# Kernel optimization log

Hardware: AMD Instinct MI355X
Metric: run time of the kernel (lower is better)

The kernel has to match this reference:

```python
import jax, jax.numpy as jnp
import numpy as np

N = 8192      # num nodes
E = 8192      # num hyperedges
D = 256       # embedding dim
DENSITY = 0.01
LEAKY = 0.2   # negative_slope of LeakyReLU


def setup_inputs() -> dict:
    key = jax.random.key(0)
    k1, k2, k3, k4, k5 = jax.random.split(key, 5)
    # sparse adjacency matrices represented densely (values * bernoulli mask)
    inp_adj = jax.random.normal(k1, (E, N), dtype=jnp.float32) * (
        jax.random.uniform(k2, (E, N)) < DENSITY
    ).astype(jnp.float32)
    att_adj = jax.random.normal(k3, (N, E), dtype=jnp.float32) * (
        jax.random.uniform(k4, (N, E)) < DENSITY
    ).astype(jnp.float32)
    embs = jax.random.normal(k5, (N, D), dtype=jnp.float32)
    return {"inp_adj": inp_adj, "att_adj": att_adj, "embs": embs}


def reference(inp_adj, att_adj, embs):
    # adj = att_adj @ inp_adj  (spgemm in the original)  -> [N, N]
    adj = att_adj @ inp_adj
    # adj @ (adj.T @ embs)  (two spmm)  -> [N, D]
    out = adj @ (adj.T @ embs)
    # LeakyReLU(negative_slope=LEAKY)
    return jnp.where(out > 0, out, LEAKY * out)
```

## Files before the change

kernel.cpp:

```cpp
#include <hip/hip_runtime.h>
#include <stdint.h>

#define NROWS 8192
#define NCOLS 8192
#define DDIM  256
#define SLOTS 160
#define SCRN  192
#define CAP   786432
#define HB    128
#define RPB   (NROWS / HB)

__device__ __forceinline__ float bf16lo(uint32_t u) { return __uint_as_float(u << 16); }
__device__ __forceinline__ float bf16hi(uint32_t u) { return __uint_as_float(u & 0xffff0000u); }
__device__ __forceinline__ uint32_t f2bf(float f) {
    uint32_t b = __float_as_uint(f);
    return (b + 0x7fffu + ((b >> 16) & 1u)) >> 16;
}

__global__ __launch_bounds__(256) void cvt_kernel(const float* __restrict__ in,
                                                  uint32_t* __restrict__ out) {
    int i = blockIdx.x * 256 + threadIdx.x;
    float2 f = ((const float2*)in)[i];
    out[i] = f2bf(f.x) | (f2bf(f.y) << 16);
}

__device__ __forceinline__ void emit_nz(float v, uint32_t col, int& base,
                                        uint2* __restrict__ s) {
    unsigned long long m = __ballot(v != 0.f);
    if (m) {
        if (v != 0.f) {
            int pre = __builtin_amdgcn_mbcnt_hi((uint32_t)(m >> 32),
                      __builtin_amdgcn_mbcnt_lo((uint32_t)m, 0u));
            int o = base + pre;
            if (o < SCRN) s[o] = make_uint2(col, __float_as_uint(v));
        }
        base += (int)__popcll(m);
    }
}

template<int CH>
__device__ __forceinline__ void process_chunk(const float4 (&d)[8], int lane,
                                              int& base, uint2* __restrict__ s) {
    #pragma unroll
    for (int i = 0; i < 8; ++i) {
        const uint32_t cbase = (uint32_t)((CH * 512 + i * 64 + lane) * 4);
        emit_nz(d[i].x, cbase + 0, base, s);
        emit_nz(d[i].y, cbase + 1, base, s);
        emit_nz(d[i].z, cbase + 2, base, s);
        emit_nz(d[i].w, cbase + 3, base, s);
    }
}

__global__ __launch_bounds__(256) void extract_kernel(
        const float* __restrict__ MA, const float* __restrict__ MB,
        int* __restrict__ rcA, uint2* __restrict__ pairA,
        int* __restrict__ rcB, uint2* __restrict__ pairB) {
    __shared__ uint2 scr[4][SCRN];
    const int wv   = threadIdx.x >> 6;
    const int lane = threadIdx.x & 63;
    const int W = blockIdx.x * 4 + wv;
    const int which = W >> 13;
    const int r = W & (NROWS - 1);
    const float* __restrict__ M = which ? MB : MA;
    int*   rc     = which ? rcB : rcA;
    uint2* g_pair = which ? pairB : pairA;

    const float4* __restrict__ M4 = (const float4*)(M + (size_t)r * NCOLS);
    uint2* __restrict__ dst = g_pair + (size_t)r * SLOTS;
    uint2* __restrict__ s = scr[wv];

    float4 da[8], db[8];
    #pragma unroll
    for (int i = 0; i < 8; ++i) da[i] = M4[0 * 512 + i * 64 + lane];
    #pragma unroll
    for (int i = 0; i < 8; ++i) db[i] = M4[1 * 512 + i * 64 + lane];
    __builtin_amdgcn_sched_barrier(0);

    int base = 0;
    process_chunk<0>(da, lane, base, s);
    #pragma unroll
    for (int i = 0; i < 8; ++i) da[i] = M4[2 * 512 + i * 64 + lane];
    __builtin_amdgcn_sched_barrier(0);
    process_chunk<1>(db, lane, base, s);
    #pragma unroll
    for (int i = 0; i < 8; ++i) db[i] = M4[3 * 512 + i * 64 + lane];
    __builtin_amdgcn_sched_barrier(0);
    process_chunk<2>(da, lane, base, s);
    process_chunk<3>(db, lane, base, s);

    const int n = base < SLOTS ? base : SLOTS;
    for (int j = lane; j < n; j += 64) dst[j] = s[j];
    if (lane == 0) rc[r] = n;
}

__global__ __launch_bounds__(256) void hist_kernel(
        const int* __restrict__ rcA, const uint2* __restrict__ pairA, int* __restrict__ PA,
        const int* __restrict__ rcB, const uint2* __restrict__ pairB, int* __restrict__ PB) {
    const int which = blockIdx.x >> 7;
    const int b = blockIdx.x & (HB - 1);
    const int* rc      = which ? rcB : rcA;
    const uint2* pair  = which ? pairB : pairA;
    int* P = which ? PB : PA;
    __shared__ int h[NCOLS];
    const int tid = threadIdx.x;
    const int wv = tid >> 6, lane = tid & 63;
    for (int i = tid; i < NCOLS; i += 256) h[i] = 0;
    __syncthreads();
    for (int r = b * RPB + wv; r < (b + 1) * RPB; r += 4) {
        const int c = rc[r];
        const uint2* __restrict__ p = pair + (size_t)r * SLOTS;
        for (int j = lane; j < c; j += 64) atomicAdd(&h[p[j].x], 1);
    }
    __syncthreads();
    for (int i = tid; i < NCOLS; i += 256) P[b * NCOLS + i] = h[i];
}

__global__ __launch_bounds__(256) void coltot_kernel(
        const int* __restrict__ PA, int* __restrict__ totA,
        const int* __restrict__ PB, int* __restrict__ totB) {
    const int which = blockIdx.x >> 5;
    const int cb = blockIdx.x & 31;
    const int* P = which ? PB : PA;
    int* tot = which ? totB : totA;
    const int c = cb * 256 + threadIdx.x;
    int sum = 0;
    #pragma unroll 8
    for (int b = 0; b < HB; ++b) sum += P[b * NCOLS + c];
    tot[c] = sum;
}

__global__ __launch_bounds__(256) void prefix_kernel(
        const int* __restrict__ totA, int* __restrict__ startA,
        const int* __restrict__ totB, int* __restrict__ startB) {
    const int* cnt = blockIdx.x ? totB : totA;
    int* start     = blockIdx.x ? startB : startA;
    __shared__ int wtot[4];
    const int tid = threadIdx.x;
    const int wv = tid >> 6, lane = tid & 63;
    const int chunk = NCOLS / 256;
    const int base = tid * chunk;
    int sum = 0;
    for (int i = 0; i < chunk; ++i) sum += cnt[base + i];
    int inc = sum;
    #pragma unroll
    for (int sd = 1; sd < 64; sd <<= 1) {
        int t = __shfl_up(inc, sd, 64);
        if (lane >= sd) inc += t;
    }
    if (lane == 63) wtot[wv] = inc;
    __syncthreads();
    if (tid == 0) {
        int acc = 0;
        #pragma unroll
        for (int i = 0; i < 4; ++i) { int t = wtot[i]; wtot[i] = acc; acc += t; }
    }
    __syncthreads();
    int run = wtot[wv] + inc - sum;
    for (int i = 0; i < chunk; ++i) { start[base + i] = run; run += cnt[base + i]; }
}

__global__ __launch_bounds__(256) void offsets_kernel(
        int* __restrict__ PA, const int* __restrict__ startA,
        int* __restrict__ PB, const int* __restrict__ startB) {
    const int which = blockIdx.x >> 5;
    const int cb = blockIdx.x & 31;
    int* P = which ? PB : PA;
    const int* start = which ? startB : startA;
    const int c = cb * 256 + threadIdx.x;
    int run = start[c];
    for (int b = 0; b < HB; ++b) {
        int t = P[b * NCOLS + c];
        P[b * NCOLS + c] = run;
        run += t;
    }
}

__global__ __launch_bounds__(256) void scatter_kernel(
        const int* __restrict__ rcA, const uint2* __restrict__ pairA,
        const int* __restrict__ PA, uint2* __restrict__ cscA,
        const int* __restrict__ rcB, const uint2* __restrict__ pairB,
        const int* __restrict__ PB, uint2* __restrict__ cscB) {
    const int which = blockIdx.x >> 7;
    const int b = blockIdx.x & (HB - 1);
    const int* rc     = which ? rcB : rcA;
    const uint2* pair = which ? pairB : pairA;
    const int* P      = which ? PB : PA;
    uint2* csc        = which ? cscB : cscA;
    __shared__ int cur[NCOLS];
    const int tid = threadIdx.x;
    const int wv = tid >> 6, lane = tid & 63;
    for (int i = tid; i < NCOLS; i += 256) cur[i] = P[b * NCOLS + i];
    __syncthreads();
    for (int r = b * RPB + wv; r < (b + 1) * RPB; r += 4) {
        const int c = rc[r];
        const uint2* __restrict__ p = pair + (size_t)r * SLOTS;
        for (int j = lane; j < c; j += 64) {
            uint2 e = p[j];
            int slot = atomicAdd(&cur[e.x], 1);
            csc[slot] = make_uint2((uint32_t)r, e.y);
        }
    }
}

struct Acc8 { float a0, a1, a2, a3, a4, a5, a6, a7; };

__device__ __forceinline__ void fma8(Acc8& a, float v, uint4 t) {
    a.a0 = fmaf(v, bf16lo(t.x), a.a0); a.a1 = fmaf(v, bf16hi(t.x), a.a1);
    a.a2 = fmaf(v, bf16lo(t.y), a.a2); a.a3 = fmaf(v, bf16hi(t.y), a.a3);
    a.a4 = fmaf(v, bf16lo(t.z), a.a4); a.a5 = fmaf(v, bf16hi(t.z), a.a5);
    a.a6 = fmaf(v, bf16lo(t.w), a.a6); a.a7 = fmaf(v, bf16hi(t.w), a.a7);
}

template<int FINAL>
__global__ __launch_bounds__(256) void spmm_kernel(
        const int* __restrict__ start, const int* __restrict__ cnt,
        const uint2* __restrict__ pairs,
        const uint4* __restrict__ X,
        void* __restrict__ Y, int fixed_stride) {
    const int wv   = threadIdx.x >> 6;
    const int lane = threadIdx.x & 63;
    const int half = lane >> 5, sub = lane & 31;
    const int r = blockIdx.x * 4 + wv;
    const int c = cnt[r];
    const uint2* __restrict__ P = pairs + (fixed_stride ? (size_t)r * SLOTS : (size_t)start[r]);
    Acc8 a = {0.f, 0.f, 0.f, 0.f, 0.f, 0.f, 0.f, 0.f};
    int j = 0;
    for (; j + 15 < c; j += 16) {
        uint2 p[8];
        uint4 x[8];
        #pragma unroll
        for (int t = 0; t < 8; ++t) p[t] = P[j + 2 * t + half];
        #pragma unroll
        for (int t = 0; t < 8; ++t) x[t] = X[(size_t)p[t].x * 32 + sub];
        #pragma unroll
        for (int t = 0; t < 8; ++t) fma8(a, __uint_as_float(p[t].y), x[t]);
    }
    for (; j + 1 < c; j += 2) {
        uint2 p = P[j + half];
        uint4 x = X[(size_t)p.x * 32 + sub];
        fma8(a, __uint_as_float(p.y), x);
    }
    if (j < c) {
        uint2 p = P[j];
        uint4 x = X[(size_t)p.x * 32 + sub];
        float v = half ? 0.f : __uint_as_float(p.y);
        fma8(a, v, x);
    }
    a.a0 += __shfl_xor(a.a0, 32); a.a1 += __shfl_xor(a.a1, 32);
    a.a2 += __shfl_xor(a.a2, 32); a.a3 += __shfl_xor(a.a3, 32);
    a.a4 += __shfl_xor(a.a4, 32); a.a5 += __shfl_xor(a.a5, 32);
    a.a6 += __shfl_xor(a.a6, 32); a.a7 += __shfl_xor(a.a7, 32);
    if (half == 0) {
        if (FINAL) {
            a.a0 = a.a0 > 0.f ? a.a0 : 0.2f * a.a0; a.a1 = a.a1 > 0.f ? a.a1 : 0.2f * a.a1;
            a.a2 = a.a2 > 0.f ? a.a2 : 0.2f * a.a2; a.a3 = a.a3 > 0.f ? a.a3 : 0.2f * a.a3;
            a.a4 = a.a4 > 0.f ? a.a4 : 0.2f * a.a4; a.a5 = a.a5 > 0.f ? a.a5 : 0.2f * a.a5;
            a.a6 = a.a6 > 0.f ? a.a6 : 0.2f * a.a6; a.a7 = a.a7 > 0.f ? a.a7 : 0.2f * a.a7;
            float4* Y4 = (float4*)Y;
            Y4[(size_t)r * 64 + sub * 2]     = make_float4(a.a0, a.a1, a.a2, a.a3);
            Y4[(size_t)r * 64 + sub * 2 + 1] = make_float4(a.a4, a.a5, a.a6, a.a7);
        } else {
            uint4 o;
            o.x = f2bf(a.a0) | (f2bf(a.a1) << 16);
            o.y = f2bf(a.a2) | (f2bf(a.a3) << 16);
            o.z = f2bf(a.a4) | (f2bf(a.a5) << 16);
            o.w = f2bf(a.a6) | (f2bf(a.a7) << 16);
            ((uint4*)Y)[(size_t)r * 32 + sub] = o;
        }
    }
}

extern "C" void kernel_launch(void* const* d_in, const int* in_sizes, int n_in,
                              void* d_out, int out_size, void* d_ws, size_t ws_size,
                              hipStream_t stream) {
    const float* Bm   = (const float*)d_in[0];
    const float* Am   = (const float*)d_in[1];
    const float* embs = (const float*)d_in[2];
    float* out = (float*)d_out;

    char* w = (char*)d_ws;
    auto alloc = [&](size_t bytes) -> char* {
        char* p = w;
        w += (bytes + 255) & ~(size_t)255;
        return p;
    };
    uint32_t* embs16 = (uint32_t*)alloc((size_t)NROWS * DDIM * 2);
    uint32_t* t1     = (uint32_t*)alloc((size_t)NROWS * DDIM * 2);
    uint32_t* t2     = (uint32_t*)alloc((size_t)NROWS * DDIM * 2);
    uint32_t* t3     = t1;

    int* rcA       = (int*)alloc(NROWS * 4);
    int* rcB       = (int*)alloc(NROWS * 4);
    int* coltotA   = (int*)alloc(NCOLS * 4);
    int* colstartA = (int*)alloc(NCOLS * 4);
    int* coltotB   = (int*)alloc(NCOLS * 4);
    int* colstartB = (int*)alloc(NCOLS * 4);
    int* PA        = (int*)alloc((size_t)HB * NCOLS * 4);
    int* PB        = (int*)alloc((size_t)HB * NCOLS * 4);

    uint2* csrA = (uint2*)alloc((size_t)NROWS * SLOTS * 8);
    uint2* csrB = (uint2*)alloc((size_t)NROWS * SLOTS * 8);
    uint2* cscA = (uint2*)alloc((size_t)CAP * 8);
    uint2* cscB = (uint2*)alloc((size_t)CAP * 8);

    cvt_kernel<<<(NROWS * DDIM / 2) / 256, 256, 0, stream>>>(embs, embs16);
    extract_kernel<<<2 * NROWS / 4, 256, 0, stream>>>(Am, Bm, rcA, csrA, rcB, csrB);
    hist_kernel<<<2 * HB, 256, 0, stream>>>(rcA, csrA, PA, rcB, csrB, PB);
    coltot_kernel<<<64, 256, 0, stream>>>(PA, coltotA, PB, coltotB);
    prefix_kernel<<<2, 256, 0, stream>>>(coltotA, colstartA, coltotB, colstartB);
    offsets_kernel<<<64, 256, 0, stream>>>(PA, colstartA, PB, colstartB);
    scatter_kernel<<<2 * HB, 256, 0, stream>>>(rcA, csrA, PA, cscA, rcB, csrB, PB, cscB);
    spmm_kernel<0><<<NROWS / 4, 256, 0, stream>>>(colstartA, coltotA, cscA, (const uint4*)embs16, t1, 0);
    spmm_kernel<0><<<NROWS / 4, 256, 0, stream>>>(colstartB, coltotB, cscB, (const uint4*)t1, t2, 0);
    spmm_kernel<0><<<NROWS / 4, 256, 0, stream>>>(nullptr, rcB, csrB, (const uint4*)t2, t3, 1);
    spmm_kernel<1><<<NROWS / 4, 256, 0, stream>>>(nullptr, rcA, csrA, (const uint4*)t3, out, 1);

    (void)in_sizes; (void)n_in; (void)out_size; (void)ws_size;
}
```

Measured before the change: 685.1 us.

## Stream dense rows into LDS with double-buffered async loads in persistent extract

The nonzero-extraction kernel becomes a persistent grid of 1024 single-wave blocks. Each wave walks 16 rows in half-row pieces, staging each piece into a double-buffered LDS area with global_load_lds and waiting on vmcnt so the next piece loads while the current one is scanned. This aims to keep more bytes in flight and free registers during the bandwidth-bound pass over the two dense 8192x8192 matrices. The trade-off is only 4 waves per CU and manual waitcnt handling, which leaves less latency hiding if the async copies stall.

Measured after the change: 714.1 us. 4.2% more time.

```diff
diff --git a/kernel.cpp b/kernel.cpp
--- a/kernel.cpp
+++ b/kernel.cpp
@@ -22,6 +22,12 @@
     int i = blockIdx.x * 256 + threadIdx.x;
     float2 f = ((const float2*)in)[i];
     out[i] = f2bf(f.x) | (f2bf(f.y) << 16);
+}
+
+__device__ __forceinline__ void gld_lds16(const float* g, float* l) {
+    __builtin_amdgcn_global_load_lds(
+        (const __attribute__((address_space(1))) void*)g,
+        (__attribute__((address_space(3))) void*)l, 16, 0, 0);
 }
 
 __device__ __forceinline__ void emit_nz(float v, uint32_t col, int& base,
@@ -38,59 +44,58 @@
     }
 }
 
-template<int CH>
-__device__ __forceinline__ void process_chunk(const float4 (&d)[8], int lane,
-                                              int& base, uint2* __restrict__ s) {
-    #pragma unroll
-    for (int i = 0; i < 8; ++i) {
-        const uint32_t cbase = (uint32_t)((CH * 512 + i * 64 + lane) * 4);
-        emit_nz(d[i].x, cbase + 0, base, s);
-        emit_nz(d[i].y, cbase + 1, base, s);
-        emit_nz(d[i].z, cbase + 2, base, s);
-        emit_nz(d[i].w, cbase + 3, base, s);
-    }
-}
-
-__global__ __launch_bounds__(256) void extract_kernel(
+__global__ __launch_bounds__(64) void extract_kernel(
         const float* __restrict__ MA, const float* __restrict__ MB,
         int* __restrict__ rcA, uint2* __restrict__ pairA,
         int* __restrict__ rcB, uint2* __restrict__ pairB) {
-    __shared__ uint2 scr[4][SCRN];
-    const int wv   = threadIdx.x >> 6;
-    const int lane = threadIdx.x & 63;
-    const int W = blockIdx.x * 4 + wv;
-    const int which = W >> 13;
-    const int r = W & (NROWS - 1);
-    const float* __restrict__ M = which ? MB : MA;
-    int*   rc     = which ? rcB : rcA;
-    uint2* g_pair = which ? pairB : pairA;
-
-    const float4* __restrict__ M4 = (const float4*)(M + (size_t)r * NCOLS);
-    uint2* __restrict__ dst = g_pair + (size_t)r * SLOTS;
-    uint2* __restrict__ s = scr[wv];
-
-    float4 da[8], db[8];
-    #pragma unroll
-    for (int i = 0; i < 8; ++i) da[i] = M4[0 * 512 + i * 64 + lane];
-    #pragma unroll
-    for (int i = 0; i < 8; ++i) db[i] = M4[1 * 512 + i * 64 + lane];
-    __builtin_amdgcn_sched_barrier(0);
+    __shared__ float stage[2][4096];
+    __shared__ uint2 scr[SCRN];
+    const int lane = threadIdx.x;
+    const int W = blockIdx.x;
+    const int H = 32;
+
+    auto issue = [&](int h, int buf) {
+        const int rg = W + (h >> 1) * 1024;
+        const float* __restrict__ M = (rg >> 13) ? MB : MA;
+        const int r = rg & (NROWS - 1);
+        const float* src = M + (size_t)r * NCOLS + (h & 1) * 4096 + lane * 4;
+        float* lp = stage[buf];
+        #pragma unroll
+        for (int k = 0; k < 16; ++k) gld_lds16(src + k * 256, lp + k * 256);
+    };
+
+    issue(0, 0);
+    issue(1, 1);
 
     int base = 0;
-    process_chunk<0>(da, lane, base, s);
-    #pragma unroll
-    for (int i = 0; i < 8; ++i) da[i] = M4[2 * 512 + i * 64 + lane];
-    __builtin_amdgcn_sched_barrier(0);
-    process_chunk<1>(db, lane, base, s);
-    #pragma unroll
-    for (int i = 0; i < 8; ++i) db[i] = M4[3 * 512 + i * 64 + lane];
-    __builtin_amdgcn_sched_barrier(0);
-    process_chunk<2>(da, lane, base, s);
-    process_chunk<3>(db, lane, base, s);
-
-    const int n = base < SLOTS ? base : SLOTS;
-    for (int j = lane; j < n; j += 64) dst[j] = s[j];
-    if (lane == 0) rc[r] = n;
+    for (int h = 0; h < H; ++h) {
+        if (h < H - 1) { asm volatile("s_waitcnt vmcnt(16)" ::: "memory"); }
+        else           { asm volatile("s_waitcnt vmcnt(0)"  ::: "memory"); }
+        __builtin_amdgcn_sched_barrier(0);
+        const float4* __restrict__ L = (const float4*)stage[h & 1];
+        const uint32_t cb0 = (uint32_t)(((h & 1) * 1024 + lane) * 4);
+        #pragma unroll
+        for (int k = 0; k < 16; ++k) {
+            float4 v = L[k * 64 + lane];
+            const uint32_t cb = cb0 + (uint32_t)(k * 256);
+            emit_nz(v.x, cb + 0, base, scr);
+            emit_nz(v.y, cb + 1, base, scr);
+            emit_nz(v.z, cb + 2, base, scr);
+            emit_nz(v.w, cb + 3, base, scr);
+        }
+        if (h & 1) {
+            const int rg = W + (h >> 1) * 1024;
+            const int which = rg >> 13;
+            const int r = rg & (NROWS - 1);
+            uint2* __restrict__ dst = (which ? pairB : pairA) + (size_t)r * SLOTS;
+            int* rc = which ? rcB : rcA;
+            const int n = base < SLOTS ? base : SLOTS;
+            for (int j = lane; j < n; j += 64) dst[j] = scr[j];
+            if (lane == 0) rc[r] = n;
+            base = 0;
+        }
+        if (h + 2 < H) issue(h + 2, h & 1);
+    }
 }
 
 __global__ __launch_bounds__(256) void hist_kernel(
@@ -304,7 +309,7 @@
     uint2* cscB = (uint2*)alloc((size_t)CAP * 8);
 
     cvt_kernel<<<(NROWS * DDIM / 2) / 256, 256, 0, stream>>>(embs, embs16);
-    extract_kernel<<<2 * NROWS / 4, 256, 0, stream>>>(Am, Bm, rcA, csrA, rcB, csrB);
+    extract_kernel<<<1024, 64, 0, stream>>>(Am, Bm, rcA, csrA, rcB, csrB);
     hist_kernel<<<2 * HB, 256, 0, stream>>>(rcA, csrA, PA, rcB, csrB, PB);
     coltot_kernel<<<64, 256, 0, stream>>>(PA, coltotA, PB, coltotB);
     prefix_kernel<<<2, 256, 0, stream>>>(coltotA, colstartA, coltotB, colstartB);
```

## Replace blocked histogram CSR-to-CSC transpose with global atomic counting and scatter

Applied to the files above, without the earlier changes.

Drops the per-block histogram, column-total and offset passes, which worked on 128x8192 partial-count arrays. Column counts are now taken with global atomics inside the extract kernel, the prefix kernel also seeds a cursor array, and the scatter runs one wave per row using global atomic slot claims. Pair loads in the scatter and SpMM kernels become nontemporal loads and stores. This cuts several launches and the partial-count traffic, in exchange for global atomic contention. Entries within each CSC column now land in nondeterministic order, so float summation order can change from run to run.

New measurement: 720.6 us. 5.2% more time.

```diff
diff --git a/kernel.cpp b/kernel.cpp
--- a/kernel.cpp
+++ b/kernel.cpp
@@ -7,8 +7,6 @@
 #define SLOTS 160
 #define SCRN  192
 #define CAP   786432
-#define HB    128
-#define RPB   (NROWS / HB)
 
 __device__ __forceinline__ float bf16lo(uint32_t u) { return __uint_as_float(u << 16); }
 __device__ __forceinline__ float bf16hi(uint32_t u) { return __uint_as_float(u & 0xffff0000u); }
@@ -22,6 +20,13 @@
     int i = blockIdx.x * 256 + threadIdx.x;
     float2 f = ((const float2*)in)[i];
     out[i] = f2bf(f.x) | (f2bf(f.y) << 16);
+}
+
+__global__ __launch_bounds__(256) void zero_kernel(int* __restrict__ a,
+                                                   int* __restrict__ b) {
+    int i = blockIdx.x * 256 + threadIdx.x;
+    a[i] = 0;
+    b[i] = 0;
 }
 
 __device__ __forceinline__ void emit_nz(float v, uint32_t col, int& base,
@@ -53,8 +58,8 @@
 
 __global__ __launch_bounds__(256) void extract_kernel(
         const float* __restrict__ MA, const float* __restrict__ MB,
-        int* __restrict__ rcA, uint2* __restrict__ pairA,
-        int* __restrict__ rcB, uint2* __restrict__ pairB) {
+        int* __restrict__ rcA, uint2* __restrict__ pairA, int* __restrict__ ctA,
+        int* __restrict__ rcB, uint2* __restrict__ pairB, int* __restrict__ ctB) {
     __shared__ uint2 scr[4][SCRN];
     const int wv   = threadIdx.x >> 6;
     const int lane = threadIdx.x & 63;
@@ -64,6 +69,7 @@
     const float* __restrict__ M = which ? MB : MA;
     int*   rc     = which ? rcB : rcA;
     uint2* g_pair = which ? pairB : pairA;
+    int*   ct     = which ? ctB : ctA;
 
     const float4* __restrict__ M4 = (const float4*)(M + (size_t)r * NCOLS);
     uint2* __restrict__ dst = g_pair + (size_t)r * SLOTS;
@@ -89,51 +95,20 @@
     process_chunk<3>(db, lane, base, s);
 
     const int n = base < SLOTS ? base : SLOTS;
-    for (int j = lane; j < n; j += 64) dst[j] = s[j];
+    for (int j = lane; j < n; j += 64) {
+        uint2 e = s[j];
+        dst[j] = e;
+        atomicAdd(&ct[e.x], 1);
+    }
     if (lane == 0) rc[r] = n;
 }
 
-__global__ __launch_bounds__(256) void hist_kernel(
-        const int* __restrict__ rcA, const uint2* __restrict__ pairA, int* __restrict__ PA,
-        const int* __restrict__ rcB, const uint2* __restrict__ pairB, int* __restrict__ PB) {
-    const int which = blockIdx.x >> 7;
-    const int b = blockIdx.x & (HB - 1);
-    const int* rc      = which ? rcB : rcA;
-    const uint2* pair  = which ? pairB : pairA;
-    int* P = which ? PB : PA;
-    __shared__ int h[NCOLS];
-    const int tid = threadIdx.x;
-    const int wv = tid >> 6, lane = tid & 63;
-    for (int i = tid; i < NCOLS; i += 256) h[i] = 0;
-    __syncthreads();
-    for (int r = b * RPB + wv; r < (b + 1) * RPB; r += 4) {
-        const int c = rc[r];
-        const uint2* __restrict__ p = pair + (size_t)r * SLOTS;
-        for (int j = lane; j < c; j += 64) atomicAdd(&h[p[j].x], 1);
-    }
-    __syncthreads();
-    for (int i = tid; i < NCOLS; i += 256) P[b * NCOLS + i] = h[i];
-}
-
-__global__ __launch_bounds__(256) void coltot_kernel(
-        const int* __restrict__ PA, int* __restrict__ totA,
-        const int* __restrict__ PB, int* __restrict__ totB) {
-    const int which = blockIdx.x >> 5;
-    const int cb = blockIdx.x & 31;
-    const int* P = which ? PB : PA;
-    int* tot = which ? totB : totA;
-    const int c = cb * 256 + threadIdx.x;
-    int sum = 0;
-    #pragma unroll 8
-    for (int b = 0; b < HB; ++b) sum += P[b * NCOLS + c];
-    tot[c] = sum;
-}
-
 __global__ __launch_bounds__(256) void prefix_kernel(
-        const int* __restrict__ totA, int* __restrict__ startA,
-        const int* __restrict__ totB, int* __restrict__ startB) {
+        const int* __restrict__ totA, int* __restrict__ startA, int* __restrict__ curA,
+        const int* __restrict__ totB, int* __restrict__ startB, int* __restrict__ curB) {
     const int* cnt = blockIdx.x ? totB : totA;
     int* start     = blockIdx.x ? startB : startA;
+    int* cur       = blockIdx.x ? curB : curA;
     __shared__ int wtot[4];
     const int tid = threadIdx.x;
     const int wv = tid >> 6, lane = tid & 63;
@@ -156,49 +131,34 @@
     }
     __syncthreads();
     int run = wtot[wv] + inc - sum;
-    for (int i = 0; i < chunk; ++i) { start[base + i] = run; run += cnt[base + i]; }
-}
-
-__global__ __launch_bounds__(256) void offsets_kernel(
-        int* __restrict__ PA, const int* __restrict__ startA,
-        int* __restrict__ PB, const int* __restrict__ startB) {
-    const int which = blockIdx.x >> 5;
-    const int cb = blockIdx.x & 31;
-    int* P = which ? PB : PA;
-    const int* start = which ? startB : startA;
-    const int c = cb * 256 + threadIdx.x;
-    int run = start[c];
-    for (int b = 0; b < HB; ++b) {
-        int t = P[b * NCOLS + c];
-        P[b * NCOLS + c] = run;
-        run += t;
+    for (int i = 0; i < chunk; ++i) {
+        start[base + i] = run;
+        cur[base + i]   = run;
+        run += cnt[base + i];
     }
 }
 
 __global__ __launch_bounds__(256) void scatter_kernel(
         const int* __restrict__ rcA, const uint2* __restrict__ pairA,
-        const int* __restrict__ PA, uint2* __restrict__ cscA,
+        int* __restrict__ curA, uint2* __restrict__ cscA,
         const int* __restrict__ rcB, const uint2* __restrict__ pairB,
-        const int* __restrict__ PB, uint2* __restrict__ cscB) {
-    const int which = blockIdx.x >> 7;
-    const int b = blockIdx.x & (HB - 1);
-    const int* rc     = which ? rcB : rcA;
+        int* __restrict__ curB, uint2* __restrict__ cscB) {
+    const int wv   = threadIdx.x >> 6;
+    const int lane = threadIdx.x & 63;
+    const int W = blockIdx.x * 4 + wv;
+    const int which = W >> 13;
+    const int r = W & (NROWS - 1);
     const uint2* pair = which ? pairB : pairA;
-    const int* P      = which ? PB : PA;
+    int* cur          = which ? curB : curA;
     uint2* csc        = which ? cscB : cscA;
-    __shared__ int cur[NCOLS];
-    const int tid = threadIdx.x;
-    const int wv = tid >> 6, lane = tid & 63;
-    for (int i = tid; i < NCOLS; i += 256) cur[i] = P[b * NCOLS + i];
-    __syncthreads();
-    for (int r = b * RPB + wv; r < (b + 1) * RPB; r += 4) {
-        const int c = rc[r];
-        const uint2* __restrict__ p = pair + (size_t)r * SLOTS;
-        for (int j = lane; j < c; j += 64) {
-            uint2 e = p[j];
-            int slot = atomicAdd(&cur[e.x], 1);
-            csc[slot] = make_uint2((uint32_t)r, e.y);
-        }
+    const int c = (which ? rcB : rcA)[r];
+    const uint2* __restrict__ p = pair + (size_t)r * SLOTS;
+    for (int j = lane; j < c; j += 64) {
+        unsigned long long pv = __builtin_nontemporal_load((const unsigned long long*)&p[j]);
+        uint32_t col = (uint32_t)pv;
+        int slot = atomicAdd(&cur[col], 1);
+        unsigned long long e = (unsigned long long)r | (pv & 0xffffffff00000000ull);
+        __builtin_nontemporal_store(e, (unsigned long long*)&csc[slot]);
     }
 }
 
@@ -209,6 +169,11 @@
     a.a2 = fmaf(v, bf16lo(t.y), a.a2); a.a3 = fmaf(v, bf16hi(t.y), a.a3);
     a.a4 = fmaf(v, bf16lo(t.z), a.a4); a.a5 = fmaf(v, bf16hi(t.z), a.a5);
     a.a6 = fmaf(v, bf16lo(t.w), a.a6); a.a7 = fmaf(v, bf16hi(t.w), a.a7);
+}
+
+__device__ __forceinline__ uint2 nt_pair(const uint2* p) {
+    unsigned long long v = __builtin_nontemporal_load((const unsigned long long*)p);
+    return make_uint2((uint32_t)v, (uint32_t)(v >> 32));
 }
 
 template<int FINAL>
@@ -229,19 +194,19 @@
         uint2 p[8];
         uint4 x[8];
         #pragma unroll
-        for (int t = 0; t < 8; ++t) p[t] = P[j + 2 * t + half];
+        for (int t = 0; t < 8; ++t) p[t] = nt_pair(&P[j + 2 * t + half]);
         #pragma unroll
         for (int t = 0; t < 8; ++t) x[t] = X[(size_t)p[t].x * 32 + sub];
         #pragma unroll
         for (int t = 0; t < 8; ++t) fma8(a, __uint_as_float(p[t].y), x[t]);
     }
     for (; j + 1 < c; j += 2) {
-        uint2 p = P[j + half];
+        uint2 p = nt_pair(&P[j + half]);
         uint4 x = X[(size_t)p.x * 32 + sub];
         fma8(a, __uint_as_float(p.y), x);
     }
     if (j < c) {
-        uint2 p = P[j];
+        uint2 p = nt_pair(&P[j]);
         uint4 x = X[(size_t)p.x * 32 + sub];
         float v = half ? 0.f : __uint_as_float(p.y);
         fma8(a, v, x);
@@ -293,23 +258,24 @@
     int* rcB       = (int*)alloc(NROWS * 4);
     int* coltotA   = (int*)alloc(NCOLS * 4);
     int* colstartA = (int*)alloc(NCOLS * 4);
+    int* curA      = (int*)alloc(NCOLS * 4);
     int* coltotB   = (int*)alloc(NCOLS * 4);
     int* colstartB = (int*)alloc(NCOLS * 4);
-    int* PA        = (int*)alloc((size_t)HB * NCOLS * 4);
-    int* PB        = (int*)alloc((size_t)HB * NCOLS * 4);
+    int* curB      = (int*)alloc(NCOLS * 4);
 
     uint2* csrA = (uint2*)alloc((size_t)NROWS * SLOTS * 8);
     uint2* csrB = (uint2*)alloc((size_t)NROWS * SLOTS * 8);
     uint2* cscA = (uint2*)alloc((size_t)CAP * 8);
     uint2* cscB = (uint2*)alloc((size_t)CAP * 8);
 
+    zero_kernel<<<32, 256, 0, stream>>>(coltotA, coltotB);
     cvt_kernel<<<(NROWS * DDIM / 2) / 256, 256, 0, stream>>>(embs, embs16);
-    extract_kernel<<<2 * NROWS / 4, 256, 0, stream>>>(Am, Bm, rcA, csrA, rcB, csrB);
-    hist_kernel<<<2 * HB, 256, 0, stream>>>(rcA, csrA, PA, rcB, csrB, PB);
-    coltot_kernel<<<64, 256, 0, stream>>>(PA, coltotA, PB, coltotB);
-    prefix_kernel<<<2, 256, 0, stream>>>(coltotA, colstartA, coltotB, colstartB);
-    offsets_kernel<<<64, 256, 0, stream>>>(PA, colstartA, PB, colstartB);
-    scatter_kernel<<<2 * HB, 256, 0, stream>>>(rcA, csrA, PA, cscA, rcB, csrB, PB, cscB);
+    extract_kernel<<<2 * NROWS / 4, 256, 0, stream>>>(Am, Bm, rcA, csrA, coltotA,
+                                                      rcB, csrB, coltotB);
+    prefix_kernel<<<2, 256, 0, stream>>>(coltotA, colstartA, curA,
+                                         coltotB, colstartB, curB);
+    scatter_kernel<<<2 * NROWS / 4, 256, 0, stream>>>(rcA, csrA, curA, cscA,
+                                                      rcB, csrB, curB, cscB);
     spmm_kernel<0><<<NROWS / 4, 256, 0, stream>>>(colstartA, coltotA, cscA, (const uint4*)embs16, t1, 0);
     spmm_kernel<0><<<NROWS / 4, 256, 0, stream>>>(colstartB, coltotB, cscB, (const uint4*)t1, t2, 0);
     spmm_kernel<0><<<NROWS / 4, 256, 0, stream>>>(nullptr, rcB, csrB, (const uint4*)t2, t3, 1);
```
